# Kernel tuning notes

Hardware: AMD Instinct MI355X
Metric: run time of the kernel (lower is better)

The kernel has to match this reference:

```python
import jax, jax.numpy as jnp
import numpy as np

N, E, IN_C, OUT_C, HEADS = 50000, 800000, 256, 256, 4
C = OUT_C // HEADS  # per-head channels = 64
BN_EPS = 1e-5


def setup_inputs() -> dict:
    key = jax.random.key(0)
    ks = jax.random.split(key, 16)
    inp = {
        'x': jax.random.normal(ks[0], (N, IN_C), dtype=jnp.float32),
        'edge_index': jax.random.randint(ks[1], (2, E), 0, N, dtype=jnp.int64),
        'edge_attr': jax.random.uniform(ks[2], (E, 1), dtype=jnp.float32),
        'spatial_coords': jax.random.normal(ks[3], (N, 2), dtype=jnp.float32),
        # GATConv params
        'W_gat': jax.random.normal(ks[4], (IN_C, HEADS * C), dtype=jnp.float32) * 0.05,
        'att_src': jax.random.normal(ks[5], (HEADS, C), dtype=jnp.float32) * 0.05,
        'att_dst': jax.random.normal(ks[6], (HEADS, C), dtype=jnp.float32) * 0.05,
        'bias_gat': jnp.zeros((HEADS * C,), dtype=jnp.float32),
        # spatial_attention MLP (computed but unused by the original forward)
        'w1': jax.random.normal(ks[7], (1, 64), dtype=jnp.float32) * 0.05,
        'b1': jnp.zeros((64,), dtype=jnp.float32),
        'w2': jax.random.normal(ks[8], (64, HEADS), dtype=jnp.float32) * 0.05,
        'b2': jnp.zeros((HEADS,), dtype=jnp.float32),
        # feature_transform: Linear + BatchNorm1d (eval stats) + ReLU (+Dropout=identity)
        'w_ft': jax.random.normal(ks[9], (IN_C, OUT_C), dtype=jnp.float32) * 0.05,
        'b_ft': jnp.zeros((OUT_C,), dtype=jnp.float32),
        'bn_gamma': jnp.ones((OUT_C,), dtype=jnp.float32),
        'bn_beta': jnp.zeros((OUT_C,), dtype=jnp.float32),
        'bn_mean': jax.random.normal(ks[10], (OUT_C,), dtype=jnp.float32) * 0.01,
        'bn_var': jax.random.uniform(ks[11], (OUT_C,), dtype=jnp.float32, minval=0.5, maxval=1.5),
    }
    return inp


def _forward(x, edge_index, edge_attr, W_gat, att_src, att_dst, bias_gat,
             w1, b1, w2, b2, w_ft, b_ft, bn_gamma, bn_beta, bn_mean, bn_var):
    n = x.shape[0]
    # add self-loops (PyG GATConv default)
    loop = jnp.arange(n, dtype=edge_index.dtype)
    src = jnp.concatenate([edge_index[0], loop])
    dst = jnp.concatenate([edge_index[1], loop])

    # linear transform: [N, heads, C]
    h = (x @ W_gat).reshape(n, HEADS, C)
    a_src = jnp.einsum('nhc,hc->nh', h, att_src)  # [N, H]
    a_dst = jnp.einsum('nhc,hc->nh', h, att_dst)  # [N, H]

    # per-edge attention logits, LeakyReLU(0.2)
    alpha = jax.nn.leaky_relu(a_src[src] + a_dst[dst], negative_slope=0.2)  # [Etot, H]
    # segment softmax over incoming edges of each destination node
    amax = jax.ops.segment_max(alpha, dst, num_segments=n)
    alpha = jnp.exp(alpha - amax[dst])
    denom = jax.ops.segment_sum(alpha, dst, num_segments=n)
    alpha = alpha / (denom[dst] + 1e-16)

    # weighted message aggregation
    msg = h[src] * alpha[:, :, None]                        # [Etot, H, C]
    agg = jax.ops.segment_sum(msg, dst, num_segments=n)     # [N, H, C]
    gat_out = agg.reshape(n, HEADS * C) + bias_gat

    # spatial attention weights (computed but UNUSED, matching original)
    spatial_weights = jax.nn.sigmoid(jax.nn.relu(edge_attr @ w1 + b1) @ w2 + b2)
    del spatial_weights

    # feature_transform (BatchNorm in eval mode, Dropout identity)
    y = x @ w_ft + b_ft
    y = (y - bn_mean) * jax.lax.rsqrt(bn_var + BN_EPS) * bn_gamma + bn_beta
    transformed = jax.nn.relu(y)

    return gat_out + transformed


def reference(x, edge_index, edge_attr, spatial_coords, W_gat, att_src, att_dst,
              bias_gat, w1, b1, w2, b2, w_ft, b_ft, bn_gamma, bn_beta, bn_mean, bn_var):
    # spatial_coords is accepted but unused by the original module's forward
    return _forward(x, edge_index, edge_attr, W_gat, att_src, att_dst, bias_gat,
                    w1, b1, w2, b2, w_ft, b_ft, bn_gamma, bn_beta, bn_mean, bn_var)
```

## Files before the change

### kernel.cpp

```cpp
#include <hip/hip_runtime.h>
#include <math.h>

typedef __attribute__((ext_vector_type(4))) float  f32x4;
typedef __attribute__((ext_vector_type(8))) short  short8;
typedef __attribute__((ext_vector_type(4))) unsigned short usx4;
typedef __attribute__((ext_vector_type(8))) unsigned short usx8;

__device__ __forceinline__ float bf2f(unsigned short u) {
    union { unsigned int i; float f; } c; c.i = ((unsigned int)u) << 16; return c.f;
}
__device__ __forceinline__ unsigned short f2bf(float f) {
    union { float f; unsigned int i; } c; c.f = f;
    unsigned int x = c.i;
    unsigned int r = (x + 0x7FFFu + ((x >> 16) & 1u)) >> 16;
    return (unsigned short)r;
}

__global__ __launch_bounds__(256) void k_convert_w(const float* __restrict__ Wg,
                                                   const float* __restrict__ Wf,
                                                   unsigned short* __restrict__ wbt) {
    int idx = blockIdx.x * blockDim.x + threadIdx.x;
    if (idx >= 512 * 256) return;
    int c = idx >> 8;
    int k = idx & 255;
    float v = (c < 256) ? Wg[k * 256 + c] : Wf[k * 256 + (c - 256)];
    wbt[idx] = f2bf(v);
}

#define BM 128
#define BN 128
#define BK 32
__global__ __launch_bounds__(256) void k_gemm(
    const float* __restrict__ x,
    const unsigned short* __restrict__ wbt,
    unsigned short* __restrict__ hb,
    unsigned short* __restrict__ tb,
    float* __restrict__ out,
    const float* __restrict__ att_s, const float* __restrict__ att_d,
    float* __restrict__ a_src, float* __restrict__ a_dst,
    const float* __restrict__ b_ft, const float* __restrict__ bn_g,
    const float* __restrict__ bn_b, const float* __restrict__ bn_m,
    const float* __restrict__ bn_v, int M) {
    __shared__ unsigned short As[BM][BK + 8];
    __shared__ unsigned short Bs[BN][BK + 8];
    const int t = threadIdx.x;
    const int w = t >> 6, lane = t & 63;
    const int wr = w >> 1, wc = w & 1;
    const int bm0 = blockIdx.y * BM;
    const int bn0 = blockIdx.x * BN;
    const int kg = lane >> 4;
    const int lm = lane & 15;

    f32x4 acc[4][4] = {};

    for (int k0 = 0; k0 < 256; k0 += BK) {
        f32x4 a0[2], a1[2];
        usx8 bv[2];
#pragma unroll
        for (int s = 0; s < 2; s++) {
            int seg = t + s * 256;
            int row = seg >> 2;
            int off = (seg & 3) * 8;
            int grow = bm0 + row; if (grow >= M) grow = M - 1;
            const float* ap = x + (long)grow * 256 + k0 + off;
            a0[s] = *(const f32x4*)ap;
            a1[s] = *(const f32x4*)(ap + 4);
            bv[s] = *(const usx8*)(wbt + (long)(bn0 + row) * 256 + k0 + off);
        }
        __syncthreads();
#pragma unroll
        for (int s = 0; s < 2; s++) {
            int seg = t + s * 256;
            int row = seg >> 2;
            int off = (seg & 3) * 8;
            usx8 av;
            av[0] = f2bf(a0[s][0]); av[1] = f2bf(a0[s][1]);
            av[2] = f2bf(a0[s][2]); av[3] = f2bf(a0[s][3]);
            av[4] = f2bf(a1[s][0]); av[5] = f2bf(a1[s][1]);
            av[6] = f2bf(a1[s][2]); av[7] = f2bf(a1[s][3]);
            *(usx8*)&As[row][off] = av;
            *(usx8*)&Bs[row][off] = bv[s];
        }
        __syncthreads();
        short8 afr[4], bfr[4];
#pragma unroll
        for (int mi = 0; mi < 4; mi++)
            afr[mi] = *(const short8*)&As[wr * 64 + mi * 16 + lm][kg * 8];
#pragma unroll
        for (int nj = 0; nj < 4; nj++)
            bfr[nj] = *(const short8*)&Bs[wc * 64 + nj * 16 + lm][kg * 8];
#pragma unroll
        for (int mi = 0; mi < 4; mi++)
#pragma unroll
            for (int nj = 0; nj < 4; nj++)
                acc[mi][nj] = __builtin_amdgcn_mfma_f32_16x16x32_bf16(
                    afr[mi], bfr[nj], acc[mi][nj], 0, 0, 0);
        __syncthreads();
    }

    const bool isH = (bn0 < 256);
#pragma unroll
    for (int mi = 0; mi < 4; mi++) {
#pragma unroll
        for (int nj = 0; nj < 4; nj++) {
            int col = bn0 + wc * 64 + nj * 16 + lm;
            f32x4 a = acc[mi][nj];
            int rowbase = bm0 + wr * 64 + mi * 16 + kg * 4;
            if (isH) {
#pragma unroll
                for (int r = 0; r < 4; r++) {
                    int row = rowbase + r;
                    if (row < M) hb[(long)row * 256 + col] = f2bf(a[r]);
                }
            } else {
                int c2 = col - 256;
                float bft = b_ft[c2], mu = bn_m[c2];
                float iv = rsqrtf(bn_v[c2] + 1e-5f);
                float g = bn_g[c2], bt = bn_b[c2];
#pragma unroll
                for (int r = 0; r < 4; r++) {
                    int row = rowbase + r;
                    if (row < M) {
                        float v = (a[r] + bft - mu) * iv * g + bt;
                        v = v > 0.f ? v : 0.f;
                        if (tb) tb[(long)row * 256 + c2] = f2bf(v);
                        else    out[(long)row * 256 + c2] = v;
                    }
                }
            }
        }
    }

    if (isH) {
        const int head = (bn0 >> 6) + wc;
        float as_c[4], ad_c[4];
#pragma unroll
        for (int nj = 0; nj < 4; nj++) {
            as_c[nj] = att_s[head * 64 + nj * 16 + lm];
            ad_c[nj] = att_d[head * 64 + nj * 16 + lm];
        }
#pragma unroll
        for (int mi = 0; mi < 4; mi++) {
#pragma unroll
            for (int r = 0; r < 4; r++) {
                float s1 = 0.f, s2 = 0.f;
#pragma unroll
                for (int nj = 0; nj < 4; nj++) {
                    s1 = fmaf(acc[mi][nj][r], as_c[nj], s1);
                    s2 = fmaf(acc[mi][nj][r], ad_c[nj], s2);
                }
#pragma unroll
                for (int o = 1; o < 16; o <<= 1) {
                    s1 += __shfl_xor(s1, o);
                    s2 += __shfl_xor(s2, o);
                }
                int row = bm0 + wr * 64 + mi * 16 + kg * 4 + r;
                if (lm == 0 && row < M) {
                    a_src[(long)row * 4 + head] = s1;
                    a_dst[(long)row * 4 + head] = s2;
                }
            }
        }
    }
}

__global__ void k_count(const int* __restrict__ ei, int* __restrict__ deg, int E) {
    int i = blockIdx.x * blockDim.x + threadIdx.x;
    if (i < E) atomicAdd(&deg[ei[E + i]], 1);
}
__global__ __launch_bounds__(256) void k_scan1(const int* __restrict__ deg,
                                               int* __restrict__ offs,
                                               int* __restrict__ bsum, int n) {
    __shared__ int tmp[256];
    int b = blockIdx.x, t = threadIdx.x;
    int base = b * 1024;
    int v[4];
#pragma unroll
    for (int j = 0; j < 4; j++) {
        int i = base + t * 4 + j;
        v[j] = (i < n) ? (deg[i] + 1) : 0;
    }
    int local = v[0] + v[1] + v[2] + v[3];
    tmp[t] = local;
    __syncthreads();
    for (int off = 1; off < 256; off <<= 1) {
        int xv = (t >= off) ? tmp[t - off] : 0;
        __syncthreads();
        tmp[t] += xv;
        __syncthreads();
    }
    int run = tmp[t] - local;
    if (t == 255) bsum[b] = tmp[255];
#pragma unroll
    for (int j = 0; j < 4; j++) {
        int i = base + t * 4 + j;
        if (i < n) offs[i] = run;
        run += v[j];
    }
}
__global__ void k_scan2(int* bsum, int nb) {
    if (threadIdx.x == 0 && blockIdx.x == 0) {
        int acc = 0;
        for (int i = 0; i < nb; i++) { int x = bsum[i]; bsum[i] = acc; acc += x; }
    }
}
__global__ void k_scan3(int* __restrict__ offs, const int* __restrict__ bsum,
                        int* __restrict__ srcs, int n) {
    int i = blockIdx.x * blockDim.x + threadIdx.x;
    if (i < n) {
        int o = offs[i] + bsum[i >> 10];
        offs[i] = o;
        srcs[o] = i;
    }
}
__global__ void k_scatter(const int* __restrict__ ei, const int* __restrict__ offs,
                          int* __restrict__ cursor, int* __restrict__ srcs, int E) {
    int i = blockIdx.x * blockDim.x + threadIdx.x;
    if (i >= E) return;
    int d = ei[E + i];
    int pos = atomicAdd(&cursor[d], 1);
    srcs[offs[d] + 1 + pos] = ei[i];
}

__global__ __launch_bounds__(256, 4) void k_agg(
    const int* __restrict__ offs, const int* __restrict__ srcs,
    const unsigned short* __restrict__ hb,
    const float* __restrict__ a_src, const float* __restrict__ a_dst,
    const float* __restrict__ bias_gat, const unsigned short* __restrict__ tb,
    float* __restrict__ out, int N, int E) {
    const int n = (blockIdx.x * 256 + threadIdx.x) >> 6;
    const int l = threadIdx.x & 63;
    if (n >= N) return;
    const int head = l >> 4;
    const int sub = l & 15;
    const int beg = offs[n];
    const int end = (n + 1 < N) ? offs[n + 1] : (E + N);
    const uint2* hp = (const uint2*)hb + l;

    const float ad = a_dst[(long)n * 4 + head];
    f32x4 acc = {};
    float den = 0.f;

    for (int base = beg; base < end; base += 16) {
        const int len = min(16, end - base);
        int sv = 0;
        float wsel = 0.f;
        if (base + sub < end) {
            sv = srcs[base + sub];
            float lv = a_src[(long)sv * 4 + head] + ad;
            lv = fmaxf(lv, 0.2f * lv);
            wsel = __expf(lv);
        }

#define AGG_EDGE(i)                                                        \
        {                                                                  \
            int src = __shfl(sv, (i));                                     \
            float wgt = __shfl(wsel, (l & 48) + (i));                      \
            uint2 hv = hp[src << 6];                                       \
            den += wgt;                                                    \
            acc[0] = fmaf(wgt, __uint_as_float(hv.x << 16), acc[0]);       \
            acc[1] = fmaf(wgt, __uint_as_float(hv.x & 0xFFFF0000u), acc[1]);\
            acc[2] = fmaf(wgt, __uint_as_float(hv.y << 16), acc[2]);       \
            acc[3] = fmaf(wgt, __uint_as_float(hv.y & 0xFFFF0000u), acc[3]);\
        }

        if (len == 16) {
#pragma unroll
            for (int i = 0; i < 16; ++i) AGG_EDGE(i)
        } else {
            for (int i = 0; i < len; ++i) AGG_EDGE(i)
        }
#undef AGG_EDGE
    }

    const float inv = 1.f / (den + 1e-16f);
    const float4 bv = ((const float4*)bias_gat)[l];
    float4 trf;
    const long rowoff = ((long)n << 8) + l * 4;
    if (tb) {
        uint2 tv = ((const uint2*)(tb + ((long)n << 8)))[l];
        trf.x = __uint_as_float(tv.x << 16);
        trf.y = __uint_as_float(tv.x & 0xFFFF0000u);
        trf.z = __uint_as_float(tv.y << 16);
        trf.w = __uint_as_float(tv.y & 0xFFFF0000u);
    } else {
        trf = *(const float4*)(out + rowoff);
    }
    float4 r;
    r.x = acc[0] * inv + bv.x + trf.x;
    r.y = acc[1] * inv + bv.y + trf.y;
    r.z = acc[2] * inv + bv.z + trf.z;
    r.w = acc[3] * inv + bv.w + trf.w;
    *(float4*)(out + rowoff) = r;
}

extern "C" void kernel_launch(void* const* d_in, const int* in_sizes, int n_in,
                              void* d_out, int out_size, void* d_ws, size_t ws_size,
                              hipStream_t stream) {
    const float* x        = (const float*)d_in[0];
    const int*   ei       = (const int*)d_in[1];
    const float* W_gat    = (const float*)d_in[4];
    const float* att_src  = (const float*)d_in[5];
    const float* att_dst  = (const float*)d_in[6];
    const float* bias_gat = (const float*)d_in[7];
    const float* w_ft     = (const float*)d_in[12];
    const float* b_ft     = (const float*)d_in[13];
    const float* bn_g     = (const float*)d_in[14];
    const float* bn_b     = (const float*)d_in[15];
    const float* bn_m     = (const float*)d_in[16];
    const float* bn_v     = (const float*)d_in[17];
    float* out = (float*)d_out;

    const int N = in_sizes[0] / 256;
    const int E = in_sizes[1] / 2;
    const int ETOT = E + N;

    char* p = (char*)d_ws;
    char* pend = p + ws_size;
    auto alloc = [&](size_t bytes) {
        void* r = (void*)p;
        p += (bytes + 255) & ~(size_t)255;
        return r;
    };
    unsigned short* wbt  = (unsigned short*)alloc((size_t)512 * 256 * 2);
    unsigned short* hb   = (unsigned short*)alloc((size_t)N * 256 * 2);
    float* a_src = (float*)alloc((size_t)N * 4 * 4);
    float* a_dst = (float*)alloc((size_t)N * 4 * 4);
    char* z0 = p;
    int* deg    = (int*)alloc((size_t)N * 4);
    int* cursor = (int*)alloc((size_t)N * 4);
    char* z1 = p;
    int* offs   = (int*)alloc((size_t)(N + 1) * 4);
    int* bsum   = (int*)alloc((size_t)256 * 4);
    int* srcs   = (int*)alloc((size_t)ETOT * 4);
    unsigned short* tb = (unsigned short*)alloc((size_t)N * 256 * 2);
    if (p > pend) tb = nullptr;

    k_convert_w<<<(512 * 256 + 255) / 256, 256, 0, stream>>>(W_gat, w_ft, wbt);

    dim3 gg(4, (N + BM - 1) / BM);
    k_gemm<<<gg, 256, 0, stream>>>(x, wbt, hb, tb, out, att_src, att_dst,
                                   a_src, a_dst, b_ft, bn_g, bn_b, bn_m, bn_v, N);

    hipMemsetAsync(z0, 0, (size_t)(z1 - z0), stream);
    k_count<<<(E + 255) / 256, 256, 0, stream>>>(ei, deg, E);
    int nb = (N + 1023) / 1024;
    k_scan1<<<nb, 256, 0, stream>>>(deg, offs, bsum, N);
    k_scan2<<<1, 64, 0, stream>>>(bsum, nb);
    k_scan3<<<(N + 255) / 256, 256, 0, stream>>>(offs, bsum, srcs, N);
    k_scatter<<<(E + 255) / 256, 256, 0, stream>>>(ei, offs, cursor, srcs, E);

    k_agg<<<(N * 64 + 255) / 256, 256, 0, stream>>>(offs, srcs, hb, a_src, a_dst,
                                                    bias_gat, tb, out, N, E);
}
```

Measured before the change: 265.7 us.

## Pre-convert x to bf16 and load GEMM tiles via direct global-to-LDS

Adds a kernel that converts x to bf16 once, then a new GEMM that streams bf16 tiles straight into shared memory with global_load_lds, using an XOR-swizzled layout, BK=64 and an occupancy hint. The aim is to halve the A-operand traffic each of the four column blocks rereads, and to skip the register staging and per-tile conversion. In exchange it adds a conversion pass (read fp32 x, write bf16) and a workspace buffer, and falls back to the old GEMM if the workspace is too small.

```diff
diff --git a/kernel.cpp b/kernel.cpp
--- a/kernel.cpp
+++ b/kernel.cpp
@@ -14,6 +14,19 @@
     unsigned int x = c.i;
     unsigned int r = (x + 0x7FFFu + ((x >> 16) & 1u)) >> 16;
     return (unsigned short)r;
+}
+
+__global__ __launch_bounds__(256) void k_convert_x(const float* __restrict__ x,
+                                                   unsigned short* __restrict__ xb,
+                                                   long total8) {
+    long i = (long)blockIdx.x * blockDim.x + threadIdx.x;
+    if (i >= total8) return;
+    const f32x4* p = (const f32x4*)x;
+    f32x4 v0 = p[2 * i], v1 = p[2 * i + 1];
+    usx8 o;
+    o[0] = f2bf(v0[0]); o[1] = f2bf(v0[1]); o[2] = f2bf(v0[2]); o[3] = f2bf(v0[3]);
+    o[4] = f2bf(v1[0]); o[5] = f2bf(v1[1]); o[6] = f2bf(v1[2]); o[7] = f2bf(v1[3]);
+    ((usx8*)xb)[i] = o;
 }
 
 __global__ __launch_bounds__(256) void k_convert_w(const float* __restrict__ Wg,
@@ -29,12 +42,147 @@
 
 #define BM 128
 #define BN 128
-#define BK 32
-__global__ __launch_bounds__(256) void k_gemm(
-    const float* __restrict__ x,
+
+__global__ __launch_bounds__(256, 4) void k_gemm_fast(
+    const unsigned short* __restrict__ xb,
     const unsigned short* __restrict__ wbt,
     unsigned short* __restrict__ hb,
     unsigned short* __restrict__ tb,
+    float* __restrict__ out,
+    const float* __restrict__ att_s, const float* __restrict__ att_d,
+    float* __restrict__ a_src, float* __restrict__ a_dst,
+    const float* __restrict__ b_ft, const float* __restrict__ bn_g,
+    const float* __restrict__ bn_b, const float* __restrict__ bn_m,
+    const float* __restrict__ bn_v, int M) {
+    __shared__ unsigned short As[128 * 64];
+    __shared__ unsigned short Bs[128 * 64];
+    const int t = threadIdx.x;
+    const int w = t >> 6, l = t & 63;
+    const int wr = w >> 1, wc = w & 1;
+    const int bm0 = blockIdx.y * BM;
+    const int bn0 = blockIdx.x * BN;
+    const int kg = l >> 4;
+    const int lm = l & 15;
+
+    const int srow = l >> 3;
+    const int scol = ((l & 7) ^ srow) << 3;
+
+    f32x4 acc[4][4] = {};
+
+    for (int kk = 0; kk < 4; kk++) {
+        const int k0 = kk * 64;
+        __syncthreads();
+#pragma unroll
+        for (int j = 0; j < 4; j++) {
+            int r = ((w * 4 + j) << 3) + srow;
+            int ga = bm0 + r; if (ga >= M) ga = M - 1;
+            __builtin_amdgcn_global_load_lds(
+                (const __attribute__((address_space(1))) unsigned int*)
+                    (xb + (long)ga * 256 + k0 + scol),
+                (__attribute__((address_space(3))) unsigned int*)
+                    (As + ((w * 4 + j) << 9)),
+                16, 0, 0);
+            __builtin_amdgcn_global_load_lds(
+                (const __attribute__((address_space(1))) unsigned int*)
+                    (wbt + (long)(bn0 + r) * 256 + k0 + scol),
+                (__attribute__((address_space(3))) unsigned int*)
+                    (Bs + ((w * 4 + j) << 9)),
+                16, 0, 0);
+        }
+        __syncthreads();
+#pragma unroll
+        for (int ks = 0; ks < 2; ks++) {
+            const int cb = (ks * 64 + kg * 16) ^ ((lm & 7) << 4);
+            short8 afr[4], bfr[4];
+#pragma unroll
+            for (int mi = 0; mi < 4; mi++) {
+                int row = wr * 64 + mi * 16 + lm;
+                afr[mi] = *(const short8*)((const char*)As + row * 128 + cb);
+            }
+#pragma unroll
+            for (int nj = 0; nj < 4; nj++) {
+                int row = wc * 64 + nj * 16 + lm;
+                bfr[nj] = *(const short8*)((const char*)Bs + row * 128 + cb);
+            }
+#pragma unroll
+            for (int mi = 0; mi < 4; mi++)
+#pragma unroll
+                for (int nj = 0; nj < 4; nj++)
+                    acc[mi][nj] = __builtin_amdgcn_mfma_f32_16x16x32_bf16(
+                        afr[mi], bfr[nj], acc[mi][nj], 0, 0, 0);
+        }
+    }
+
+    const bool isH = (bn0 < 256);
+#pragma unroll
+    for (int mi = 0; mi < 4; mi++) {
+#pragma unroll
+        for (int nj = 0; nj < 4; nj++) {
+            int col = bn0 + wc * 64 + nj * 16 + lm;
+            f32x4 a = acc[mi][nj];
+            int rowbase = bm0 + wr * 64 + mi * 16 + kg * 4;
+            if (isH) {
+#pragma unroll
+                for (int r = 0; r < 4; r++) {
+                    int row = rowbase + r;
+                    if (row < M) hb[(long)row * 256 + col] = f2bf(a[r]);
+                }
+            } else {
+                int c2 = col - 256;
+                float bft = b_ft[c2], mu = bn_m[c2];
+                float iv = rsqrtf(bn_v[c2] + 1e-5f);
+                float g = bn_g[c2], bt = bn_b[c2];
+#pragma unroll
+                for (int r = 0; r < 4; r++) {
+                    int row = rowbase + r;
+                    if (row < M) {
+                        float v = (a[r] + bft - mu) * iv * g + bt;
+                        v = v > 0.f ? v : 0.f;
+                        if (tb) tb[(long)row * 256 + c2] = f2bf(v);
+                        else    out[(long)row * 256 + c2] = v;
+                    }
+                }
+            }
+        }
+    }
+
+    if (isH) {
+        const int head = (bn0 >> 6) + wc;
+        float as_c[4], ad_c[4];
+#pragma unroll
+        for (int nj = 0; nj < 4; nj++) {
+            as_c[nj] = att_s[head * 64 + nj * 16 + lm];
+            ad_c[nj] = att_d[head * 64 + nj * 16 + lm];
+        }
+#pragma unroll
+        for (int mi = 0; mi < 4; mi++) {
+#pragma unroll
+            for (int r = 0; r < 4; r++) {
+                float s1 = 0.f, s2 = 0.f;
+#pragma unroll
+                for (int nj = 0; nj < 4; nj++) {
+                    s1 = fmaf(acc[mi][nj][r], as_c[nj], s1);
+                    s2 = fmaf(acc[mi][nj][r], ad_c[nj], s2);
+                }
+#pragma unroll
+                for (int o = 1; o < 16; o <<= 1) {
+                    s1 += __shfl_xor(s1, o);
+                    s2 += __shfl_xor(s2, o);
+                }
+                int row = bm0 + wr * 64 + mi * 16 + kg * 4 + r;
+                if (lm == 0 && row < M) {
+                    a_src[(long)row * 4 + head] = s1;
+                    a_dst[(long)row * 4 + head] = s2;
+                }
+            }
+        }
+    }
+}
+
+#define BK 32
+__global__ __launch_bounds__(256) void k_gemm(
+    const float* __restrict__ x, const unsigned short* __restrict__ wbt,
+    unsigned short* __restrict__ hb, unsigned short* __restrict__ tb,
     float* __restrict__ out,
     const float* __restrict__ att_s, const float* __restrict__ att_d,
     float* __restrict__ a_src, float* __restrict__ a_dst,
@@ -50,9 +198,7 @@
     const int bn0 = blockIdx.x * BN;
     const int kg = lane >> 4;
     const int lm = lane & 15;
-
     f32x4 acc[4][4] = {};
-
     for (int k0 = 0; k0 < 256; k0 += BK) {
         f32x4 a0[2], a1[2];
         usx8 bv[2];
@@ -97,7 +243,6 @@
                     afr[mi], bfr[nj], acc[mi][nj], 0, 0, 0);
         __syncthreads();
     }
-
     const bool isH = (bn0 < 256);
 #pragma unroll
     for (int mi = 0; mi < 4; mi++) {
@@ -130,7 +275,6 @@
             }
         }
     }
-
     if (isH) {
         const int head = (bn0 >> 6) + wc;
         float as_c[4], ad_c[4];
@@ -333,14 +477,23 @@
     int* offs   = (int*)alloc((size_t)(N + 1) * 4);
     int* bsum   = (int*)alloc((size_t)256 * 4);
     int* srcs   = (int*)alloc((size_t)ETOT * 4);
+    unsigned short* xb = (unsigned short*)alloc((size_t)N * 256 * 2);
+    if (p > pend) xb = nullptr;
     unsigned short* tb = (unsigned short*)alloc((size_t)N * 256 * 2);
     if (p > pend) tb = nullptr;
 
     k_convert_w<<<(512 * 256 + 255) / 256, 256, 0, stream>>>(W_gat, w_ft, wbt);
 
     dim3 gg(4, (N + BM - 1) / BM);
-    k_gemm<<<gg, 256, 0, stream>>>(x, wbt, hb, tb, out, att_src, att_dst,
-                                   a_src, a_dst, b_ft, bn_g, bn_b, bn_m, bn_v, N);
+    if (xb) {
+        long total8 = (long)N * 256 / 8;
+        k_convert_x<<<(int)((total8 + 255) / 256), 256, 0, stream>>>(x, xb, total8);
+        k_gemm_fast<<<gg, 256, 0, stream>>>(xb, wbt, hb, tb, out, att_src, att_dst,
+                                            a_src, a_dst, b_ft, bn_g, bn_b, bn_m, bn_v, N);
+    } else {
+        k_gemm<<<gg, 256, 0, stream>>>(x, wbt, hb, tb, out, att_src, att_dst,
+                                       a_src, a_dst, b_ft, bn_g, bn_b, bn_m, bn_v, N);
+    }
 
     hipMemsetAsync(z0, 0, (size_t)(z1 - z0), stream);
     k_count<<<(E + 255) / 256, 256, 0, stream>>>(ei, deg, E);
```

Result: faster. 235.0 us (-11.5%).
